# Performance work log

Measured on AMD Instinct MI355X. Metric: run time of the kernel, lower is better.

The kernel has to match this reference:

```python
import jax, jax.numpy as jnp
import numpy as np

STATE_DIM = 64; ACTION_DIM = 16; DET = 512; STOCH = 64; HID = 512
B = 128; T = 512


def _lin(key, out_d, in_d):
    k1, k2 = jax.random.split(key)
    lim = 1.0 / np.sqrt(in_d)
    w = jax.random.uniform(k1, (out_d, in_d), minval=-lim, maxval=lim, dtype=jnp.float32)
    b = jax.random.uniform(k2, (out_d,), minval=-lim, maxval=lim, dtype=jnp.float32)
    return w, b


def setup_inputs() -> dict:
    key = jax.random.key(0)
    ks = jax.random.split(key, 12)
    enc_w, enc_b = _lin(ks[0], HID, STATE_DIM)
    dec_w, dec_b = _lin(ks[1], STATE_DIM + 2, DET + STOCH)
    pri_enc_w, pri_enc_b = _lin(ks[2], DET, STOCH + ACTION_DIM)
    gru_wi, gru_bi = _lin(ks[3], 3 * DET, DET)
    gru_wh, gru_bh = _lin(ks[4], 3 * DET, DET)
    pri_d1_w, pri_d1_b = _lin(ks[5], HID, DET)
    pri_d2_w, pri_d2_b = _lin(ks[6], 2 * STOCH, HID)
    pos_enc_w, pos_enc_b = _lin(ks[7], HID, DET + HID)
    pos_dec_w, pos_dec_b = _lin(ks[8], 2 * STOCH, HID)
    observation = jax.random.normal(ks[9], (B, T, STATE_DIM), dtype=jnp.float32)
    actions = jax.random.normal(ks[10], (B, T, ACTION_DIM), dtype=jnp.float32)
    eps = jax.random.normal(ks[11], (B, T, STOCH), dtype=jnp.float32)
    return dict(observation=observation, actions=actions, eps=eps,
                enc_w=enc_w, enc_b=enc_b, dec_w=dec_w, dec_b=dec_b,
                pri_enc_w=pri_enc_w, pri_enc_b=pri_enc_b,
                gru_wi=gru_wi, gru_bi=gru_bi, gru_wh=gru_wh, gru_bh=gru_bh,
                pri_d1_w=pri_d1_w, pri_d1_b=pri_d1_b,
                pri_d2_w=pri_d2_w, pri_d2_b=pri_d2_b,
                pos_enc_w=pos_enc_w, pos_enc_b=pos_enc_b,
                pos_dec_w=pos_dec_w, pos_dec_b=pos_dec_b)


def reference(observation, actions, eps,
              enc_w, enc_b, dec_w, dec_b,
              pri_enc_w, pri_enc_b, gru_wi, gru_bi, gru_wh, gru_bh,
              pri_d1_w, pri_d1_b, pri_d2_w, pri_d2_b,
              pos_enc_w, pos_enc_b, pos_dec_w, pos_dec_b):
    Bsz = observation.shape[0]
    S = eps.shape[-1]
    D = gru_wh.shape[-1]
    # obs embedding: elu(Linear(obs))
    obs_emb = jax.nn.elu(jnp.einsum('bti,hi->bth', observation, enc_w) + enc_b)
    # time-major for scan
    emb_t = jnp.swapaxes(obs_emb, 0, 1)   # [T,B,H]
    act_t = jnp.swapaxes(actions, 0, 1)   # [T,B,A]
    eps_t = jnp.swapaxes(eps, 0, 1)       # [T,B,S]

    def step(carry, inp):
        stoch, det = carry                       # [B,S], [B,D]
        emb, act, e = inp
        # ---- prior: encode (stoch, action), GRU, decode to shift/scale
        x = jnp.concatenate([stoch, act], -1)
        x = jax.nn.elu(x @ pri_enc_w.T + pri_enc_b)          # [B,D]
        gi = x @ gru_wi.T + gru_bi                           # [B,3D]
        gh = det @ gru_wh.T + gru_bh
        ir, iz, ia = jnp.split(gi, 3, -1)
        hr, hz, ha = jnp.split(gh, 3, -1)
        r = jax.nn.sigmoid(ir + hr)
        z = jax.nn.sigmoid(iz + hz)
        n = jnp.tanh(ia + r * ha)
        det = (1.0 - z) * n + z * det                        # new deterministic state
        px = jax.nn.elu(det @ pri_d1_w.T + pri_d1_b)
        px = px @ pri_d2_w.T + pri_d2_b
        p_shift, p_raw = jnp.split(px, 2, -1)
        p_scale = jax.nn.softplus(p_raw) + 0.1
        # ---- posterior: encode (det, embedding) -> shift/scale
        qx = jnp.concatenate([det, emb], -1)
        qx = jax.nn.elu(qx @ pos_enc_w.T + pos_enc_b)
        qx = qx @ pos_dec_w.T + pos_dec_b
        q_shift, q_raw = jnp.split(qx, 2, -1)
        q_scale = jax.nn.softplus(q_raw) + 0.1
        # reparameterized posterior sample
        stoch = q_shift + q_scale * e
        return (stoch, det), (stoch, det, q_shift, q_scale, p_shift, p_scale)

    init = (jnp.zeros((Bsz, S), observation.dtype), jnp.zeros((Bsz, D), observation.dtype))
    _, ys = jax.lax.scan(step, init, (emb_t, act_t, eps_t))
    stochs, dets, q_sh, q_sc, p_sh, p_sc = [jnp.swapaxes(y, 0, 1) for y in ys]
    feats = jnp.concatenate([stochs, dets], -1)              # State.flatten()
    outs = jnp.einsum('btf,of->bto', feats, dec_w) + dec_b   # [B,T,state_dim+2]
    return stochs, dets, outs, q_sh, q_sc, p_sh, p_sc
```

## Files before the change

### kernel.cpp

```cpp
#include <hip/hip_runtime.h>
#include <math.h>

#define BDIM 128
#define TDIM 512
#define BT (BDIM*TDIM)

__device__ __forceinline__ float eluf(float v){ return v > 0.f ? v : expm1f(v); }
__device__ __forceinline__ float softplusf(float v){ return fmaxf(v,0.f) + log1pf(expf(-fabsf(v))); }
__device__ __forceinline__ float sigmoidf(float v){ return 1.f/(1.f+expf(-v)); }

struct GemmP {
  const float* x1; long ldx1;
  const float* x2; long ldx2;
  int split;
  const float* w; int ldw;
  const float* biask;
  const float* bias;
  float* out;  long ldo;
  float* out2;
  int M, N, K, k0;
};

enum { SRC_CONCAT=0, SRC_ELUSUM=1 };
enum { EPI_ELU=0, EPI_PLAIN=1, EPI_PARTIAL=2, EPI_PSCALE=3 };

template<int SRC, int EPI, int BM>
__global__ __launch_bounds__(256) void gemm_k(GemmP pa, GemmP pb)
{
  const GemmP p = (blockIdx.z==0) ? pa : pb;
  constexpr int TM = BM/16;
  __shared__ float  Xs[BM][16];
  __shared__ float4 Ws4[16][16];
  const int tid = threadIdx.x;
  const int nt = tid & 15;
  const int mt = tid >> 4;
  const int n0 = blockIdx.x * 64;
  const int m0 = blockIdx.y * BM;

  float acc[TM][4];
  #pragma unroll
  for (int i=0;i<TM;i++){ acc[i][0]=0.f; acc[i][1]=0.f; acc[i][2]=0.f; acc[i][3]=0.f; }

  const int ktiles = p.K / 16;
  for (int kt=0; kt<ktiles; ++kt){
    const int kbase = p.k0 + kt*16;
    {
      const int nload4 = BM*16/4;
      if (tid < nload4){
        const int mi = tid >> 2;
        const int kk = (tid & 3) * 4;
        const int kabs = kbase + kk;
        float4 v;
        if (SRC == SRC_CONCAT){
          const float* src; long row; int k2;
          if (kabs < p.split){ src = p.x1; row = (long)(m0+mi)*p.ldx1; k2 = kabs; }
          else               { src = p.x2; row = (long)(m0+mi)*p.ldx2; k2 = kabs - p.split; }
          if (src) v = *(const float4*)(src + row + k2);
          else { v.x=0.f; v.y=0.f; v.z=0.f; v.w=0.f; }
        } else {
          const long row = (long)(m0+mi)*p.ldx1;
          float4 a = *(const float4*)(p.x1 + row + kabs);
          float4 b = *(const float4*)(p.x2 + row + kabs);
          v.x = eluf(a.x + b.x + p.biask[kabs+0]);
          v.y = eluf(a.y + b.y + p.biask[kabs+1]);
          v.z = eluf(a.z + b.z + p.biask[kabs+2]);
          v.w = eluf(a.w + b.w + p.biask[kabs+3]);
        }
        *(float4*)(&Xs[mi][kk]) = v;
      }
    }
    {
      const int kk = tid >> 4;
      const int n4 = (tid & 15) * 4;
      const int n = n0 + n4;
      const long base = (long)(kbase + kk) * p.ldw + n;
      float4 v;
      if (n + 3 < p.N) v = *(const float4*)(p.w + base);
      else {
        v.x = (n+0 < p.N) ? p.w[base+0] : 0.f;
        v.y = (n+1 < p.N) ? p.w[base+1] : 0.f;
        v.z = (n+2 < p.N) ? p.w[base+2] : 0.f;
        v.w = (n+3 < p.N) ? p.w[base+3] : 0.f;
      }
      Ws4[kk][tid & 15] = v;
    }
    __syncthreads();
    #pragma unroll
    for (int kk=0; kk<16; ++kk){
      const float4 w4 = Ws4[kk][nt];
      #pragma unroll
      for (int i=0;i<TM;i++){
        const float xv = Xs[mt*TM+i][kk];
        acc[i][0] = fmaf(xv, w4.x, acc[i][0]);
        acc[i][1] = fmaf(xv, w4.y, acc[i][1]);
        acc[i][2] = fmaf(xv, w4.z, acc[i][2]);
        acc[i][3] = fmaf(xv, w4.w, acc[i][3]);
      }
    }
    __syncthreads();
  }
  #pragma unroll
  for (int i=0;i<TM;i++){
    const int m = m0 + mt*TM + i;
    #pragma unroll
    for (int j=0;j<4;j++){
      const int n = n0 + nt*4 + j;
      if (n >= p.N) continue;
      float v = acc[i][j];
      if (EPI == EPI_PARTIAL){
        p.out[(long)m*p.ldo + n] = v;
      } else if (EPI == EPI_ELU){
        p.out[(long)m*p.ldo + n] = eluf(v + p.bias[n]);
      } else if (EPI == EPI_PLAIN){
        p.out[(long)m*p.ldo + n] = v + p.bias[n];
      } else {
        v += p.bias[n];
        if (n < 64) p.out [(long)m*64 + n]      = v;
        else        p.out2[(long)m*64 + (n-64)] = softplusf(v) + 0.1f;
      }
    }
  }
}

__global__ void transpose_k(const float* __restrict__ src, float* __restrict__ dst, int R, int C){
  __shared__ float tile[32][33];
  const int c0 = blockIdx.x*32, r0 = blockIdx.y*32;
  const int tx = threadIdx.x, ty = threadIdx.y;
  for (int i=ty; i<32; i+=8){
    const int r = r0+i, c = c0+tx;
    tile[i][tx] = (r<R && c<C) ? src[(long)r*C + c] : 0.f;
  }
  __syncthreads();
  for (int i=ty; i<32; i+=8){
    const int r = r0+tx, c = c0+i;
    if (r<R && c<C) dst[(long)c*R + r] = tile[tx][i];
  }
}

__global__ void gate_k(const float* __restrict__ gi, const float* __restrict__ gh,
                       const float* __restrict__ det_prev, float* __restrict__ det_out){
  const int idx = blockIdx.x*blockDim.x + threadIdx.x;
  const int b = idx >> 9, n = idx & 511;
  const long g = (long)b*1536 + n;
  const float ir = gi[g], iz = gi[g+512], ia = gi[g+1024];
  const float hr = gh[g], hz = gh[g+512], ha = gh[g+1024];
  const float dp = det_prev ? det_prev[(long)b*TDIM*512 + n] : 0.f;
  const float r = sigmoidf(ir+hr);
  const float z = sigmoidf(iz+hz);
  const float nn = tanhf(ia + r*ha);
  det_out[(long)b*TDIM*512 + n] = (1.f - z)*nn + z*dp;
}

__global__ void stoch_k(const float* __restrict__ qa, const float* __restrict__ qb,
                        const float* __restrict__ pos_dec_b, const float* __restrict__ eps_t,
                        float* __restrict__ q_sh, float* __restrict__ q_sc, float* __restrict__ st){
  const int idx = blockIdx.x*blockDim.x + threadIdx.x;
  const int b = idx >> 6, s = idx & 63;
  const long q = (long)b*128;
  const float v0 = qa[q+s]    + qb[q+s]    + pos_dec_b[s];
  const float v1 = qa[q+64+s] + qb[q+64+s] + pos_dec_b[64+s];
  const float sc = softplusf(v1) + 0.1f;
  const float e  = eps_t[(long)b*TDIM*64 + s];
  const long o = (long)b*TDIM*64 + s;
  q_sh[o] = v0;
  q_sc[o] = sc;
  st[o]   = v0 + sc*e;
}

extern "C" void kernel_launch(void* const* d_in, const int* in_sizes, int n_in,
                              void* d_out, int out_size, void* d_ws, size_t ws_size,
                              hipStream_t stream)
{
  const float* obs       = (const float*)d_in[0];
  const float* act       = (const float*)d_in[1];
  const float* eps       = (const float*)d_in[2];
  const float* enc_w     = (const float*)d_in[3];
  const float* enc_b     = (const float*)d_in[4];
  const float* dec_w     = (const float*)d_in[5];
  const float* dec_b     = (const float*)d_in[6];
  const float* pri_enc_w = (const float*)d_in[7];
  const float* pri_enc_b = (const float*)d_in[8];
  const float* gru_wi    = (const float*)d_in[9];
  const float* gru_bi    = (const float*)d_in[10];
  const float* gru_wh    = (const float*)d_in[11];
  const float* gru_bh    = (const float*)d_in[12];
  const float* pri_d1_w  = (const float*)d_in[13];
  const float* pri_d1_b  = (const float*)d_in[14];
  const float* pri_d2_w  = (const float*)d_in[15];
  const float* pri_d2_b  = (const float*)d_in[16];
  const float* pos_enc_w = (const float*)d_in[17];
  const float* pos_enc_b = (const float*)d_in[18];
  const float* pos_dec_w = (const float*)d_in[19];
  const float* pos_dec_b = (const float*)d_in[20];

  float* out     = (float*)d_out;
  float* o_stoch = out;
  float* o_det   = o_stoch + (long)BT*64;
  float* o_outs  = o_det   + (long)BT*512;
  float* o_qsh   = o_outs  + (long)BT*66;
  float* o_qsc   = o_qsh   + (long)BT*64;
  float* o_psh   = o_qsc   + (long)BT*64;
  float* o_psc   = o_psh   + (long)BT*64;

  float* w = (float*)d_ws;
  float* enc_wT     = w; w += 64*512;
  float* pri_enc_wT = w; w += 80*512;
  float* gru_wiT    = w; w += 512*1536;
  float* gru_whT    = w; w += 512*1536;
  float* pri_d1T    = w; w += 512*512;
  float* pri_d2T    = w; w += 512*128;
  float* pos_encT   = w; w += 1024*512;
  float* pos_decT   = w; w += 512*128;
  float* dec_wT     = w; w += 576*66;
  float* emb        = w; w += (long)BT*512;
  float* x_ws       = w; w += 128*512;
  float* gi_ws      = w; w += 128*1536;
  float* gh_ws      = w; w += 128*1536;
  float* qx1a       = w; w += 128*512;
  float* qx1b       = w; w += 128*512;
  float* qa         = w; w += 128*128;
  float* qb         = w; w += 128*128;

  {
    struct { const float* s; float* d; int R, C; } tps[9] = {
      {enc_w,     enc_wT,     512, 64  },
      {pri_enc_w, pri_enc_wT, 512, 80  },
      {gru_wi,    gru_wiT,    1536,512 },
      {gru_wh,    gru_whT,    1536,512 },
      {pri_d1_w,  pri_d1T,    512, 512 },
      {pri_d2_w,  pri_d2T,    128, 512 },
      {pos_enc_w, pos_encT,   512, 1024},
      {pos_dec_w, pos_decT,   128, 512 },
      {dec_w,     dec_wT,     66,  576 },
    };
    for (int i=0;i<9;i++){
      dim3 g((tps[i].C+31)/32, (tps[i].R+31)/32), b(32,8);
      hipLaunchKernelGGL(transpose_k, g, b, 0, stream, tps[i].s, tps[i].d, tps[i].R, tps[i].C);
    }
  }

  {
    GemmP p{}; p.x1=obs; p.ldx1=64; p.split=64; p.w=enc_wT; p.ldw=512;
    p.bias=enc_b; p.out=emb; p.ldo=512; p.M=BT; p.N=512; p.K=64; p.k0=0;
    hipLaunchKernelGGL((gemm_k<SRC_CONCAT,EPI_ELU,64>), dim3(8,BT/64,1), dim3(256), 0, stream, p, p);
  }

  for (int t=0; t<TDIM; ++t){
    {
      GemmP p{};
      p.x1 = t ? (o_stoch + (long)(t-1)*64) : nullptr; p.ldx1 = (long)TDIM*64;
      p.x2 = act + (long)t*16;                         p.ldx2 = (long)TDIM*16;
      p.split = 64; p.w = pri_enc_wT; p.ldw = 512; p.bias = pri_enc_b;
      p.out = x_ws; p.ldo = 512; p.M = 128; p.N = 512; p.K = 80; p.k0 = 0;
      hipLaunchKernelGGL((gemm_k<SRC_CONCAT,EPI_ELU,16>), dim3(8,8,1), dim3(256), 0, stream, p, p);
    }
    {
      GemmP p0{}; p0.x1 = x_ws; p0.ldx1 = 512; p0.split = 512;
      p0.w = gru_wiT; p0.ldw = 1536; p0.bias = gru_bi;
      p0.out = gi_ws; p0.ldo = 1536; p0.M = 128; p0.N = 1536; p0.K = 512; p0.k0 = 0;
      GemmP p1 = p0;
      p1.x1 = t ? (o_det + (long)(t-1)*512) : nullptr; p1.ldx1 = (long)TDIM*512;
      p1.w = gru_whT; p1.bias = gru_bh; p1.out = gh_ws;
      hipLaunchKernelGGL((gemm_k<SRC_CONCAT,EPI_PLAIN,16>), dim3(24,8,2), dim3(256), 0, stream, p0, p1);
    }
    hipLaunchKernelGGL(gate_k, dim3(256), dim3(256), 0, stream,
        gi_ws, gh_ws, t ? (o_det + (long)(t-1)*512) : nullptr, o_det + (long)t*512);
    {
      GemmP p0{};
      p0.x1 = o_det + (long)t*512; p0.ldx1 = (long)TDIM*512;
      p0.x2 = emb   + (long)t*512; p0.ldx2 = (long)TDIM*512;
      p0.split = 512; p0.w = pos_encT; p0.ldw = 512;
      p0.out = qx1a; p0.ldo = 512; p0.M = 128; p0.N = 512; p0.K = 512; p0.k0 = 0;
      GemmP p1 = p0; p1.k0 = 512; p1.out = qx1b;
      hipLaunchKernelGGL((gemm_k<SRC_CONCAT,EPI_PARTIAL,16>), dim3(8,8,2), dim3(256), 0, stream, p0, p1);
    }
    {
      GemmP p0{};
      p0.x1 = qx1a; p0.ldx1 = 512; p0.x2 = qx1b; p0.ldx2 = 512; p0.biask = pos_enc_b;
      p0.w = pos_decT; p0.ldw = 128;
      p0.out = qa; p0.ldo = 128; p0.M = 128; p0.N = 128; p0.K = 256; p0.k0 = 0;
      GemmP p1 = p0; p1.k0 = 256; p1.out = qb;
      hipLaunchKernelGGL((gemm_k<SRC_ELUSUM,EPI_PARTIAL,16>), dim3(2,8,2), dim3(256), 0, stream, p0, p1);
    }
    hipLaunchKernelGGL(stoch_k, dim3(32), dim3(256), 0, stream,
        qa, qb, pos_dec_b, eps + (long)t*64,
        o_qsh + (long)t*64, o_qsc + (long)t*64, o_stoch + (long)t*64);
  }

  {
    GemmP p{}; p.x1 = o_det; p.ldx1 = 512; p.split = 512;
    p.w = pri_d1T; p.ldw = 512; p.bias = pri_d1_b;
    p.out = emb ; p.ldo = 512; p.M = BT; p.N = 512; p.K = 512; p.k0 = 0;
    hipLaunchKernelGGL((gemm_k<SRC_CONCAT,EPI_ELU,64>), dim3(8,BT/64,1), dim3(256), 0, stream, p, p);
  }
  {
    GemmP p{}; p.x1 = emb; p.ldx1 = 512; p.split = 512;
    p.w = pri_d2T; p.ldw = 128; p.bias = pri_d2_b;
    p.out = o_psh; p.out2 = o_psc; p.M = BT; p.N = 128; p.K = 512; p.k0 = 0;
    hipLaunchKernelGGL((gemm_k<SRC_CONCAT,EPI_PSCALE,64>), dim3(2,BT/64,1), dim3(256), 0, stream, p, p);
  }
  {
    GemmP p{}; p.x1 = o_stoch; p.ldx1 = 64; p.x2 = o_det; p.ldx2 = 512; p.split = 64;
    p.w = dec_wT; p.ldw = 66; p.bias = dec_b;
    p.out = o_outs; p.ldo = 66; p.M = BT; p.N = 66; p.K = 576; p.k0 = 0;
    hipLaunchKernelGGL((gemm_k<SRC_CONCAT,EPI_PLAIN,64>), dim3(2,BT/64,1), dim3(256), 0, stream, p, p);
  }
}
```

Measured before the change: 42.73 ms.

## Replace per-timestep kernel launches with a persistent cooperative scan kernel

The recurrent loop, previously six kernel launches per timestep across 512 steps, becomes one cooperative kernel of 256 workgroups. Inside it the stages are separated by grid-wide syncs. The GRU input and hidden weights are permuted so that each workgroup computes all three gates for its own 8 output columns, which fuses the gate math into the GEMM epilogue. The posterior GEMMs no longer use split-K partial buffers. This removes launch overhead and intermediate traffic, at the cost of four grid barriers per step and low per-workgroup parallelism with small tiles.

```diff
diff --git a/kernel.cpp b/kernel.cpp
--- a/kernel.cpp
+++ b/kernel.cpp
@@ -1,5 +1,8 @@
 #include <hip/hip_runtime.h>
+#include <hip/hip_cooperative_groups.h>
 #include <math.h>
+
+namespace cg = cooperative_groups;
 
 #define BDIM 128
 #define TDIM 512
@@ -137,34 +140,198 @@
   }
 }
 
-__global__ void gate_k(const float* __restrict__ gi, const float* __restrict__ gh,
-                       const float* __restrict__ det_prev, float* __restrict__ det_out){
+__global__ void gru_perm_k(const float* __restrict__ wi, const float* __restrict__ wh,
+                           float* __restrict__ wiP, float* __restrict__ whP){
   const int idx = blockIdx.x*blockDim.x + threadIdx.x;
-  const int b = idx >> 9, n = idx & 511;
-  const long g = (long)b*1536 + n;
-  const float ir = gi[g], iz = gi[g+512], ia = gi[g+1024];
-  const float hr = gh[g], hz = gh[g+512], ha = gh[g+1024];
-  const float dp = det_prev ? det_prev[(long)b*TDIM*512 + n] : 0.f;
-  const float r = sigmoidf(ir+hr);
-  const float z = sigmoidf(iz+hz);
-  const float nn = tanhf(ia + r*ha);
-  det_out[(long)b*TDIM*512 + n] = (1.f - z)*nn + z*dp;
+  if (idx >= 512*1536) return;
+  const int k = idx / 1536, np = idx - k*1536;
+  const int g = np / 24, r = np - g*24;
+  const int m = r >> 3, j = r & 7;
+  const long src = (long)(m*512 + g*8 + j)*512 + k;
+  wiP[idx] = wi[src];
+  whP[idx] = wh[src];
 }
 
-__global__ void stoch_k(const float* __restrict__ qa, const float* __restrict__ qb,
-                        const float* __restrict__ pos_dec_b, const float* __restrict__ eps_t,
-                        float* __restrict__ q_sh, float* __restrict__ q_sc, float* __restrict__ st){
-  const int idx = blockIdx.x*blockDim.x + threadIdx.x;
-  const int b = idx >> 6, s = idx & 63;
-  const long q = (long)b*128;
-  const float v0 = qa[q+s]    + qb[q+s]    + pos_dec_b[s];
-  const float v1 = qa[q+64+s] + qb[q+64+s] + pos_dec_b[64+s];
-  const float sc = softplusf(v1) + 0.1f;
-  const float e  = eps_t[(long)b*TDIM*64 + s];
-  const long o = (long)b*TDIM*64 + s;
-  q_sh[o] = v0;
-  q_sc[o] = sc;
-  st[o]   = v0 + sc*e;
+struct ScanP {
+  const float* act;
+  const float* eps;
+  const float* emb;
+  const float* priW;
+  const float* pri_b;
+  const float* wiP;
+  const float* whP;
+  const float* gbi;
+  const float* gbh;
+  const float* posW;
+  const float* pos_b;
+  const float* pdW;
+  const float* pd_b;
+  float* x_ws;
+  float* qx_ws;
+  float* o_stoch;
+  float* o_det;
+  float* o_qsh;
+  float* o_qsc;
+};
+
+__global__ __launch_bounds__(256) void scan_k(ScanP p)
+{
+  cg::grid_group grid = cg::this_grid();
+  const int wg  = blockIdx.x;
+  const int tid = threadIdx.x;
+  const int b8  = tid >> 3;
+  const int j8  = tid & 7;
+
+  __shared__ union {
+    struct { float X[32][84]; float W[8][84]; } a;
+    struct { float X[32][33]; float D[32][33]; float4 Wi[32][8]; float4 Wh[32][8]; } bc;
+    struct { float X[32][36]; float W[8][36]; } d;
+    struct { float X[32][36]; float W[16][36]; } e;
+  } sm;
+
+  for (int t = 0; t < TDIM; ++t){
+    {
+      const int r0 = (wg >> 6) * 32;
+      const int c0 = (wg & 63) * 8;
+      for (int i = tid; i < 32*80; i += 256){
+        const int b = i / 80, k = i - b*80;
+        float v;
+        if (k < 64) v = t ? p.o_stoch[((long)(r0+b)*TDIM + (t-1))*64 + k] : 0.f;
+        else        v = p.act[((long)(r0+b)*TDIM + t)*16 + (k-64)];
+        sm.a.X[b][k] = v;
+      }
+      for (int i = tid; i < 8*80; i += 256){
+        const int k = i >> 3, j = i & 7;
+        sm.a.W[j][k] = p.priW[(long)k*512 + c0 + j];
+      }
+      __syncthreads();
+      float acc = 0.f;
+      #pragma unroll
+      for (int k4 = 0; k4 < 20; ++k4){
+        const float4 x4 = *(const float4*)&sm.a.X[b8][k4*4];
+        const float4 w4 = *(const float4*)&sm.a.W[j8][k4*4];
+        acc = fmaf(x4.x,w4.x,acc); acc = fmaf(x4.y,w4.y,acc);
+        acc = fmaf(x4.z,w4.z,acc); acc = fmaf(x4.w,w4.w,acc);
+      }
+      p.x_ws[(long)(r0+b8)*512 + c0 + j8] = eluf(acc + p.pri_b[c0 + j8]);
+    }
+    grid.sync();
+
+    {
+      const int r0 = (wg >> 6) * 32;
+      const int g  = wg & 63;
+      const float* detp = t ? (p.o_det + (long)(t-1)*512) : nullptr;
+      float ai0=0.f, ai1=0.f, ai2=0.f, ah0=0.f, ah1=0.f, ah2=0.f;
+      for (int kt = 0; kt < 16; ++kt){
+        const int kb = kt*32;
+        for (int i = tid; i < 1024; i += 256){
+          const int b = i >> 5, kk = i & 31;
+          sm.bc.X[b][kk] = p.x_ws[(long)(r0+b)*512 + kb + kk];
+          sm.bc.D[b][kk] = detp ? detp[(long)(r0+b)*TDIM*512 + kb + kk] : 0.f;
+        }
+        for (int i = tid; i < 768; i += 256){
+          const int kk = i / 24, r = i - kk*24;
+          const int m = r >> 3, j = r & 7;
+          const long src = (long)(kb + kk)*1536 + g*24 + r;
+          ((float*)&sm.bc.Wi[kk][j])[m] = p.wiP[src];
+          ((float*)&sm.bc.Wh[kk][j])[m] = p.whP[src];
+        }
+        __syncthreads();
+        #pragma unroll
+        for (int kk = 0; kk < 32; ++kk){
+          const float xv = sm.bc.X[b8][kk];
+          const float dv = sm.bc.D[b8][kk];
+          const float4 wi = sm.bc.Wi[kk][j8];
+          const float4 wh = sm.bc.Wh[kk][j8];
+          ai0 = fmaf(xv, wi.x, ai0); ai1 = fmaf(xv, wi.y, ai1); ai2 = fmaf(xv, wi.z, ai2);
+          ah0 = fmaf(dv, wh.x, ah0); ah1 = fmaf(dv, wh.y, ah1); ah2 = fmaf(dv, wh.z, ah2);
+        }
+        __syncthreads();
+      }
+      const int c = g*8 + j8;
+      const float ir = ai0 + p.gbi[c],        hr = ah0 + p.gbh[c];
+      const float iz = ai1 + p.gbi[512 + c],  hz = ah1 + p.gbh[512 + c];
+      const float ia = ai2 + p.gbi[1024 + c], ha = ah2 + p.gbh[1024 + c];
+      const float r  = sigmoidf(ir + hr);
+      const float z  = sigmoidf(iz + hz);
+      const float nn = tanhf(ia + r*ha);
+      const float dp = detp ? detp[(long)(r0+b8)*TDIM*512 + c] : 0.f;
+      p.o_det[((long)(r0+b8)*TDIM + t)*512 + c] = (1.f - z)*nn + z*dp;
+    }
+    grid.sync();
+
+    {
+      const int r0 = (wg >> 6) * 32;
+      const int c0 = (wg & 63) * 8;
+      const float* detT = p.o_det + (long)t*512;
+      const float* embT = p.emb   + (long)t*512;
+      float acc = 0.f;
+      for (int kt = 0; kt < 32; ++kt){
+        const int kb = kt*32;
+        for (int i = tid; i < 1024; i += 256){
+          const int b = i >> 5, kk = i & 31;
+          const int k = kb + kk;
+          sm.d.X[b][kk] = (k < 512) ? detT[(long)(r0+b)*TDIM*512 + k]
+                                    : embT[(long)(r0+b)*TDIM*512 + (k-512)];
+        }
+        {
+          const int kk = tid >> 3, j = tid & 7;
+          sm.d.W[j][kk] = p.posW[(long)(kb+kk)*512 + c0 + j];
+        }
+        __syncthreads();
+        #pragma unroll
+        for (int k4 = 0; k4 < 8; ++k4){
+          const float4 x4 = *(const float4*)&sm.d.X[b8][k4*4];
+          const float4 w4 = *(const float4*)&sm.d.W[j8][k4*4];
+          acc = fmaf(x4.x,w4.x,acc); acc = fmaf(x4.y,w4.y,acc);
+          acc = fmaf(x4.z,w4.z,acc); acc = fmaf(x4.w,w4.w,acc);
+        }
+        __syncthreads();
+      }
+      p.qx_ws[(long)(r0+b8)*512 + c0 + j8] = eluf(acc + p.pos_b[c0 + j8]);
+    }
+    grid.sync();
+
+    if (wg < 32){
+      const int r0 = (wg >> 3) * 32;
+      const int c0 = (wg & 7) * 8;
+      float a0 = 0.f, a1 = 0.f;
+      for (int kt = 0; kt < 16; ++kt){
+        const int kb = kt*32;
+        for (int i = tid; i < 1024; i += 256){
+          const int b = i >> 5, kk = i & 31;
+          sm.e.X[b][kk] = p.qx_ws[(long)(r0+b)*512 + kb + kk];
+        }
+        for (int i = tid; i < 512; i += 256){
+          const int kk = i >> 4, jj = i & 15;
+          const int c = (jj < 8) ? (c0 + jj) : (64 + c0 + (jj - 8));
+          sm.e.W[jj][kk] = p.pdW[(long)(kb+kk)*128 + c];
+        }
+        __syncthreads();
+        #pragma unroll
+        for (int k4 = 0; k4 < 8; ++k4){
+          const float4 x4 = *(const float4*)&sm.e.X[b8][k4*4];
+          const float4 w0 = *(const float4*)&sm.e.W[j8][k4*4];
+          const float4 w1 = *(const float4*)&sm.e.W[8 + j8][k4*4];
+          a0 = fmaf(x4.x,w0.x,a0); a0 = fmaf(x4.y,w0.y,a0);
+          a0 = fmaf(x4.z,w0.z,a0); a0 = fmaf(x4.w,w0.w,a0);
+          a1 = fmaf(x4.x,w1.x,a1); a1 = fmaf(x4.y,w1.y,a1);
+          a1 = fmaf(x4.z,w1.z,a1); a1 = fmaf(x4.w,w1.w,a1);
+        }
+        __syncthreads();
+      }
+      const int c = c0 + j8;
+      const float v0 = a0 + p.pd_b[c];
+      const float v1 = a1 + p.pd_b[64 + c];
+      const float sc = softplusf(v1) + 0.1f;
+      const long o = ((long)(r0+b8)*TDIM + t)*64 + c;
+      const float e = p.eps[o];
+      p.o_qsh[o]   = v0;
+      p.o_qsc[o]   = sc;
+      p.o_stoch[o] = v0 + sc*e;
+    }
+    grid.sync();
+  }
 }
 
 extern "C" void kernel_launch(void* const* d_in, const int* in_sizes, int n_in,
@@ -205,8 +372,8 @@
   float* w = (float*)d_ws;
   float* enc_wT     = w; w += 64*512;
   float* pri_enc_wT = w; w += 80*512;
-  float* gru_wiT    = w; w += 512*1536;
-  float* gru_whT    = w; w += 512*1536;
+  float* gru_wiP    = w; w += 512*1536;
+  float* gru_whP    = w; w += 512*1536;
   float* pri_d1T    = w; w += 512*512;
   float* pri_d2T    = w; w += 512*128;
   float* pos_encT   = w; w += 1024*512;
@@ -214,29 +381,24 @@
   float* dec_wT     = w; w += 576*66;
   float* emb        = w; w += (long)BT*512;
   float* x_ws       = w; w += 128*512;
-  float* gi_ws      = w; w += 128*1536;
-  float* gh_ws      = w; w += 128*1536;
-  float* qx1a       = w; w += 128*512;
-  float* qx1b       = w; w += 128*512;
-  float* qa         = w; w += 128*128;
-  float* qb         = w; w += 128*128;
-
-  {
-    struct { const float* s; float* d; int R, C; } tps[9] = {
+  float* qx_ws      = w; w += 128*512;
+
+  {
+    struct { const float* s; float* d; int R, C; } tps[7] = {
       {enc_w,     enc_wT,     512, 64  },
       {pri_enc_w, pri_enc_wT, 512, 80  },
-      {gru_wi,    gru_wiT,    1536,512 },
-      {gru_wh,    gru_whT,    1536,512 },
       {pri_d1_w,  pri_d1T,    512, 512 },
       {pri_d2_w,  pri_d2T,    128, 512 },
       {pos_enc_w, pos_encT,   512, 1024},
       {pos_dec_w, pos_decT,   128, 512 },
       {dec_w,     dec_wT,     66,  576 },
     };
-    for (int i=0;i<9;i++){
+    for (int i=0;i<7;i++){
       dim3 g((tps[i].C+31)/32, (tps[i].R+31)/32), b(32,8);
       hipLaunchKernelGGL(transpose_k, g, b, 0, stream, tps[i].s, tps[i].d, tps[i].R, tps[i].C);
     }
+    hipLaunchKernelGGL(gru_perm_k, dim3((512*1536+255)/256), dim3(256), 0, stream,
+                       gru_wi, gru_wh, gru_wiP, gru_whP);
   }
 
   {
@@ -245,46 +407,17 @@
     hipLaunchKernelGGL((gemm_k<SRC_CONCAT,EPI_ELU,64>), dim3(8,BT/64,1), dim3(256), 0, stream, p, p);
   }
 
-  for (int t=0; t<TDIM; ++t){
-    {
-      GemmP p{};
-      p.x1 = t ? (o_stoch + (long)(t-1)*64) : nullptr; p.ldx1 = (long)TDIM*64;
-      p.x2 = act + (long)t*16;                         p.ldx2 = (long)TDIM*16;
-      p.split = 64; p.w = pri_enc_wT; p.ldw = 512; p.bias = pri_enc_b;
-      p.out = x_ws; p.ldo = 512; p.M = 128; p.N = 512; p.K = 80; p.k0 = 0;
-      hipLaunchKernelGGL((gemm_k<SRC_CONCAT,EPI_ELU,16>), dim3(8,8,1), dim3(256), 0, stream, p, p);
-    }
-    {
-      GemmP p0{}; p0.x1 = x_ws; p0.ldx1 = 512; p0.split = 512;
-      p0.w = gru_wiT; p0.ldw = 1536; p0.bias = gru_bi;
-      p0.out = gi_ws; p0.ldo = 1536; p0.M = 128; p0.N = 1536; p0.K = 512; p0.k0 = 0;
-      GemmP p1 = p0;
-      p1.x1 = t ? (o_det + (long)(t-1)*512) : nullptr; p1.ldx1 = (long)TDIM*512;
-      p1.w = gru_whT; p1.bias = gru_bh; p1.out = gh_ws;
-      hipLaunchKernelGGL((gemm_k<SRC_CONCAT,EPI_PLAIN,16>), dim3(24,8,2), dim3(256), 0, stream, p0, p1);
-    }
-    hipLaunchKernelGGL(gate_k, dim3(256), dim3(256), 0, stream,
-        gi_ws, gh_ws, t ? (o_det + (long)(t-1)*512) : nullptr, o_det + (long)t*512);
-    {
-      GemmP p0{};
-      p0.x1 = o_det + (long)t*512; p0.ldx1 = (long)TDIM*512;
-      p0.x2 = emb   + (long)t*512; p0.ldx2 = (long)TDIM*512;
-      p0.split = 512; p0.w = pos_encT; p0.ldw = 512;
-      p0.out = qx1a; p0.ldo = 512; p0.M = 128; p0.N = 512; p0.K = 512; p0.k0 = 0;
-      GemmP p1 = p0; p1.k0 = 512; p1.out = qx1b;
-      hipLaunchKernelGGL((gemm_k<SRC_CONCAT,EPI_PARTIAL,16>), dim3(8,8,2), dim3(256), 0, stream, p0, p1);
-    }
-    {
-      GemmP p0{};
-      p0.x1 = qx1a; p0.ldx1 = 512; p0.x2 = qx1b; p0.ldx2 = 512; p0.biask = pos_enc_b;
-      p0.w = pos_decT; p0.ldw = 128;
-      p0.out = qa; p0.ldo = 128; p0.M = 128; p0.N = 128; p0.K = 256; p0.k0 = 0;
-      GemmP p1 = p0; p1.k0 = 256; p1.out = qb;
-      hipLaunchKernelGGL((gemm_k<SRC_ELUSUM,EPI_PARTIAL,16>), dim3(2,8,2), dim3(256), 0, stream, p0, p1);
-    }
-    hipLaunchKernelGGL(stoch_k, dim3(32), dim3(256), 0, stream,
-        qa, qb, pos_dec_b, eps + (long)t*64,
-        o_qsh + (long)t*64, o_qsc + (long)t*64, o_stoch + (long)t*64);
+  {
+    ScanP p;
+    p.act = act; p.eps = eps; p.emb = emb;
+    p.priW = pri_enc_wT; p.pri_b = pri_enc_b;
+    p.wiP = gru_wiP; p.whP = gru_whP; p.gbi = gru_bi; p.gbh = gru_bh;
+    p.posW = pos_encT; p.pos_b = pos_enc_b;
+    p.pdW = pos_decT;  p.pd_b = pos_dec_b;
+    p.x_ws = x_ws; p.qx_ws = qx_ws;
+    p.o_stoch = o_stoch; p.o_det = o_det; p.o_qsh = o_qsh; p.o_qsc = o_qsc;
+    void* args[] = { &p };
+    hipLaunchCooperativeKernel((const void*)scan_k, dim3(256), dim3(256), args, 0, stream);
   }
 
   {
```

Result: slower. 147.2 ms (+244.6%).

## Fuse GRU gate into posterior GEMM and merge stoch with next-step prior encoder

Applied to the files above, without the earlier changes.

Cuts the per-timestep launch count from six to three. The GRU gate is computed while loading the posterior-encoder GEMM operand, and one block column writes det out. A new kernel fuses the pos_dec GEMM, the stoch sampling and the next step's prior-encoder GEMM, so the qa/qb buffers and the separate gate and stoch kernels go away. The cost is redundant gate computation across the eight N-blocks and a small 16-block grid for the fused tail kernel, which limits parallelism.

```diff
diff --git a/kernel.cpp b/kernel.cpp
--- a/kernel.cpp
+++ b/kernel.cpp
@@ -12,6 +12,7 @@
 struct GemmP {
   const float* x1; long ldx1;
   const float* x2; long ldx2;
+  const float* x3;
   int split;
   const float* w; int ldw;
   const float* biask;
@@ -21,7 +22,7 @@
   int M, N, K, k0;
 };
 
-enum { SRC_CONCAT=0, SRC_ELUSUM=1 };
+enum { SRC_CONCAT=0, SRC_ELUSUM=1, SRC_GATE=2 };
 enum { EPI_ELU=0, EPI_PLAIN=1, EPI_PARTIAL=2, EPI_PSCALE=3 };
 
 template<int SRC, int EPI, int BM>
@@ -44,7 +45,27 @@
   const int ktiles = p.K / 16;
   for (int kt=0; kt<ktiles; ++kt){
     const int kbase = p.k0 + kt*16;
-    {
+    if (SRC == SRC_GATE){
+      const int mi = tid >> 4;
+      const int kk = tid & 15;
+      const int kabs = kbase + kk;
+      float xv;
+      if (kabs < p.split){
+        const long g = (long)(m0+mi)*p.ldx1 + kabs;
+        const float ir = p.x1[g], iz = p.x1[g+512], ia = p.x1[g+1024];
+        const float hr = p.x2[g], hz = p.x2[g+512], ha = p.x2[g+1024];
+        const float dp = p.x3 ? p.x3[(long)(m0+mi)*TDIM*512 + kabs] : 0.f;
+        const float r  = sigmoidf(ir+hr);
+        const float z  = sigmoidf(iz+hz);
+        const float nn = tanhf(ia + r*ha);
+        xv = (1.f - z)*nn + z*dp;
+        if (blockIdx.x==0 && p.out2)
+          p.out2[(long)(m0+mi)*TDIM*512 + kabs] = xv;
+      } else {
+        xv = p.x1[(long)(m0+mi)*p.ldx1 + (kabs - 512)];
+      }
+      Xs[mi][kk] = xv;
+    } else {
       const int nload4 = BM*16/4;
       if (tid < nload4){
         const int mi = tid >> 2;
@@ -137,34 +158,108 @@
   }
 }
 
-__global__ void gate_k(const float* __restrict__ gi, const float* __restrict__ gh,
-                       const float* __restrict__ det_prev, float* __restrict__ det_out){
-  const int idx = blockIdx.x*blockDim.x + threadIdx.x;
-  const int b = idx >> 9, n = idx & 511;
-  const long g = (long)b*1536 + n;
-  const float ir = gi[g], iz = gi[g+512], ia = gi[g+1024];
-  const float hr = gh[g], hz = gh[g+512], ha = gh[g+1024];
-  const float dp = det_prev ? det_prev[(long)b*TDIM*512 + n] : 0.f;
-  const float r = sigmoidf(ir+hr);
-  const float z = sigmoidf(iz+hz);
-  const float nn = tanhf(ia + r*ha);
-  det_out[(long)b*TDIM*512 + n] = (1.f - z)*nn + z*dp;
-}
-
-__global__ void stoch_k(const float* __restrict__ qa, const float* __restrict__ qb,
-                        const float* __restrict__ pos_dec_b, const float* __restrict__ eps_t,
-                        float* __restrict__ q_sh, float* __restrict__ q_sc, float* __restrict__ st){
-  const int idx = blockIdx.x*blockDim.x + threadIdx.x;
-  const int b = idx >> 6, s = idx & 63;
-  const long q = (long)b*128;
-  const float v0 = qa[q+s]    + qb[q+s]    + pos_dec_b[s];
-  const float v1 = qa[q+64+s] + qb[q+64+s] + pos_dec_b[64+s];
-  const float sc = softplusf(v1) + 0.1f;
-  const float e  = eps_t[(long)b*TDIM*64 + s];
-  const long o = (long)b*TDIM*64 + s;
-  q_sh[o] = v0;
-  q_sc[o] = sc;
-  st[o]   = v0 + sc*e;
+struct EP {
+  const float* qx1a;
+  const float* qx1b;
+  const float* biask;
+  const float* pdW;
+  const float* pd_b;
+  const float* eps_t;
+  const float* act_next;
+  const float* priW;
+  const float* pri_b;
+  float* o_qsh; float* o_qsc; float* o_stoch;
+  float* x_ws;
+};
+
+__global__ __launch_bounds__(256) void e_k(EP p)
+{
+  __shared__ float  Xs[8][16];
+  __shared__ float4 Ws4[16][32];
+  __shared__ float  Q[8][132];
+  __shared__ float  X2[8][84];
+  __shared__ float4 W2[80][32];
+  const int tid = threadIdx.x;
+  const int r0 = blockIdx.x * 8;
+  const int mt = tid >> 5;
+  const int nt = tid & 31;
+
+  float a0=0.f, a1=0.f, a2=0.f, a3=0.f;
+  for (int kt=0; kt<32; ++kt){
+    const int kb = kt*16;
+    if (tid < 32){
+      const int mi = tid >> 2, kk = (tid & 3)*4;
+      const long row = (long)(r0+mi)*512 + kb + kk;
+      float4 a = *(const float4*)(p.qx1a + row);
+      float4 b = *(const float4*)(p.qx1b + row);
+      float4 v;
+      v.x = eluf(a.x + b.x + p.biask[kb+kk+0]);
+      v.y = eluf(a.y + b.y + p.biask[kb+kk+1]);
+      v.z = eluf(a.z + b.z + p.biask[kb+kk+2]);
+      v.w = eluf(a.w + b.w + p.biask[kb+kk+3]);
+      *(float4*)&Xs[mi][kk] = v;
+    }
+    {
+      const int r = tid >> 5, c4 = tid & 31;
+      Ws4[r][c4]   = *(const float4*)(p.pdW + (long)(kb+r)*128   + c4*4);
+      Ws4[r+8][c4] = *(const float4*)(p.pdW + (long)(kb+r+8)*128 + c4*4);
+    }
+    __syncthreads();
+    #pragma unroll
+    for (int kk=0; kk<16; ++kk){
+      const float x = Xs[mt][kk];
+      const float4 w = Ws4[kk][nt];
+      a0 = fmaf(x, w.x, a0); a1 = fmaf(x, w.y, a1);
+      a2 = fmaf(x, w.z, a2); a3 = fmaf(x, w.w, a3);
+    }
+    __syncthreads();
+  }
+  Q[mt][nt*4+0]=a0; Q[mt][nt*4+1]=a1; Q[mt][nt*4+2]=a2; Q[mt][nt*4+3]=a3;
+  __syncthreads();
+
+  for (int i=tid; i<8*64; i+=256){
+    const int r = i>>6, c = i&63;
+    const float v0 = Q[r][c]    + p.pd_b[c];
+    const float v1 = Q[r][64+c] + p.pd_b[64+c];
+    const float sc = softplusf(v1) + 0.1f;
+    const long o = (long)(r0+r)*TDIM*64 + c;
+    const float st = v0 + sc*p.eps_t[o];
+    p.o_qsh[o]   = v0;
+    p.o_qsc[o]   = sc;
+    p.o_stoch[o] = st;
+    X2[r][c] = st;
+  }
+
+  if (p.act_next){
+    for (int i=tid; i<8*16; i+=256){
+      const int r = i>>4, c = i&15;
+      X2[r][64+c] = p.act_next[(long)(r0+r)*TDIM*16 + c];
+    }
+    __syncthreads();
+    for (int cc=0; cc<4; ++cc){
+      const int c0 = cc*128;
+      for (int i=tid; i<80*32; i+=256){
+        const int k = i>>5, n4 = i&31;
+        W2[k][n4] = *(const float4*)(p.priW + (long)k*512 + c0 + n4*4);
+      }
+      __syncthreads();
+      float b0=0.f, b1=0.f, b2=0.f, b3=0.f;
+      #pragma unroll
+      for (int k=0; k<80; ++k){
+        const float x = X2[mt][k];
+        const float4 w = W2[k][nt];
+        b0 = fmaf(x, w.x, b0); b1 = fmaf(x, w.y, b1);
+        b2 = fmaf(x, w.z, b2); b3 = fmaf(x, w.w, b3);
+      }
+      const int c = c0 + nt*4;
+      float* o = p.x_ws + (long)(r0+mt)*512 + c;
+      o[0] = eluf(b0 + p.pri_b[c+0]);
+      o[1] = eluf(b1 + p.pri_b[c+1]);
+      o[2] = eluf(b2 + p.pri_b[c+2]);
+      o[3] = eluf(b3 + p.pri_b[c+3]);
+      __syncthreads();
+    }
+  }
 }
 
 extern "C" void kernel_launch(void* const* d_in, const int* in_sizes, int n_in,
@@ -218,8 +313,6 @@
   float* gh_ws      = w; w += 128*1536;
   float* qx1a       = w; w += 128*512;
   float* qx1b       = w; w += 128*512;
-  float* qa         = w; w += 128*128;
-  float* qb         = w; w += 128*128;
 
   {
     struct { const float* s; float* d; int R, C; } tps[9] = {
@@ -245,46 +338,56 @@
     hipLaunchKernelGGL((gemm_k<SRC_CONCAT,EPI_ELU,64>), dim3(8,BT/64,1), dim3(256), 0, stream, p, p);
   }
 
+  {
+    GemmP p{};
+    p.x1 = nullptr; p.ldx1 = (long)TDIM*64;
+    p.x2 = act;     p.ldx2 = (long)TDIM*16;
+    p.split = 64; p.w = pri_enc_wT; p.ldw = 512; p.bias = pri_enc_b;
+    p.out = x_ws; p.ldo = 512; p.M = 128; p.N = 512; p.K = 80; p.k0 = 0;
+    hipLaunchKernelGGL((gemm_k<SRC_CONCAT,EPI_ELU,16>), dim3(8,8,1), dim3(256), 0, stream, p, p);
+  }
+
   for (int t=0; t<TDIM; ++t){
-    {
-      GemmP p{};
-      p.x1 = t ? (o_stoch + (long)(t-1)*64) : nullptr; p.ldx1 = (long)TDIM*64;
-      p.x2 = act + (long)t*16;                         p.ldx2 = (long)TDIM*16;
-      p.split = 64; p.w = pri_enc_wT; p.ldw = 512; p.bias = pri_enc_b;
-      p.out = x_ws; p.ldo = 512; p.M = 128; p.N = 512; p.K = 80; p.k0 = 0;
-      hipLaunchKernelGGL((gemm_k<SRC_CONCAT,EPI_ELU,16>), dim3(8,8,1), dim3(256), 0, stream, p, p);
-    }
+    const float* det_prev = t ? (o_det + (long)(t-1)*512) : nullptr;
     {
       GemmP p0{}; p0.x1 = x_ws; p0.ldx1 = 512; p0.split = 512;
       p0.w = gru_wiT; p0.ldw = 1536; p0.bias = gru_bi;
       p0.out = gi_ws; p0.ldo = 1536; p0.M = 128; p0.N = 1536; p0.K = 512; p0.k0 = 0;
       GemmP p1 = p0;
-      p1.x1 = t ? (o_det + (long)(t-1)*512) : nullptr; p1.ldx1 = (long)TDIM*512;
+      p1.x1 = det_prev; p1.ldx1 = (long)TDIM*512;
       p1.w = gru_whT; p1.bias = gru_bh; p1.out = gh_ws;
       hipLaunchKernelGGL((gemm_k<SRC_CONCAT,EPI_PLAIN,16>), dim3(24,8,2), dim3(256), 0, stream, p0, p1);
     }
-    hipLaunchKernelGGL(gate_k, dim3(256), dim3(256), 0, stream,
-        gi_ws, gh_ws, t ? (o_det + (long)(t-1)*512) : nullptr, o_det + (long)t*512);
     {
       GemmP p0{};
-      p0.x1 = o_det + (long)t*512; p0.ldx1 = (long)TDIM*512;
-      p0.x2 = emb   + (long)t*512; p0.ldx2 = (long)TDIM*512;
-      p0.split = 512; p0.w = pos_encT; p0.ldw = 512;
-      p0.out = qx1a; p0.ldo = 512; p0.M = 128; p0.N = 512; p0.K = 512; p0.k0 = 0;
-      GemmP p1 = p0; p1.k0 = 512; p1.out = qx1b;
-      hipLaunchKernelGGL((gemm_k<SRC_CONCAT,EPI_PARTIAL,16>), dim3(8,8,2), dim3(256), 0, stream, p0, p1);
+      p0.x1 = gi_ws; p0.ldx1 = 1536;
+      p0.x2 = gh_ws; p0.ldx2 = 1536;
+      p0.x3 = det_prev;
+      p0.split = 512;
+      p0.w = pos_encT; p0.ldw = 512;
+      p0.out = qx1a; p0.ldo = 512; p0.out2 = o_det + (long)t*512;
+      p0.M = 128; p0.N = 512; p0.K = 512; p0.k0 = 0;
+      GemmP p1{};
+      p1.x1 = emb + (long)t*512; p1.ldx1 = (long)TDIM*512;
+      p1.split = 0;
+      p1.w = pos_encT; p1.ldw = 512;
+      p1.out = qx1b; p1.ldo = 512; p1.out2 = nullptr;
+      p1.M = 128; p1.N = 512; p1.K = 512; p1.k0 = 512;
+      hipLaunchKernelGGL((gemm_k<SRC_GATE,EPI_PARTIAL,16>), dim3(8,8,2), dim3(256), 0, stream, p0, p1);
     }
     {
-      GemmP p0{};
-      p0.x1 = qx1a; p0.ldx1 = 512; p0.x2 = qx1b; p0.ldx2 = 512; p0.biask = pos_enc_b;
-      p0.w = pos_decT; p0.ldw = 128;
-      p0.out = qa; p0.ldo = 128; p0.M = 128; p0.N = 128; p0.K = 256; p0.k0 = 0;
-      GemmP p1 = p0; p1.k0 = 256; p1.out = qb;
-      hipLaunchKernelGGL((gemm_k<SRC_ELUSUM,EPI_PARTIAL,16>), dim3(2,8,2), dim3(256), 0, stream, p0, p1);
-    }
-    hipLaunchKernelGGL(stoch_k, dim3(32), dim3(256), 0, stream,
-        qa, qb, pos_dec_b, eps + (long)t*64,
-        o_qsh + (long)t*64, o_qsc + (long)t*64, o_stoch + (long)t*64);
+      EP p;
+      p.qx1a = qx1a; p.qx1b = qx1b; p.biask = pos_enc_b;
+      p.pdW = pos_decT; p.pd_b = pos_dec_b;
+      p.eps_t = eps + (long)t*64;
+      p.act_next = (t+1 < TDIM) ? (act + (long)(t+1)*16) : nullptr;
+      p.priW = pri_enc_wT; p.pri_b = pri_enc_b;
+      p.o_qsh = o_qsh + (long)t*64;
+      p.o_qsc = o_qsc + (long)t*64;
+      p.o_stoch = o_stoch + (long)t*64;
+      p.x_ws = x_ws;
+      hipLaunchKernelGGL(e_k, dim3(16), dim3(256), 0, stream, p);
+    }
   }
 
   {
```

New measurement: 68.14 ms. 59.5% more time.
